# Optimization experiments

Measured on AMD Instinct MI355X. Metric: run time of the kernel, lower is better.

## Reference

```python
import jax, jax.numpy as jnp
import numpy as np

EPS = 1e-6  # flax.linen.LayerNorm default

def layer_norm(x, scale, bias):
    mean = jnp.mean(x, axis=-1, keepdims=True)
    var = jnp.mean(jnp.square(x - mean), axis=-1, keepdims=True)
    return (x - mean) * jax.lax.rsqrt(var + EPS) * scale + bias

def setup_inputs() -> dict:
    key = jax.random.key(0)
    ks = jax.random.split(key, 4)
    B, P, D, H = 2, 2048, 768, 12
    hd = D // H
    x = jax.random.normal(ks[0], (B, P, D), dtype=jnp.float32)
    W_qkv = jax.random.normal(ks[1], (D, 3 * D), dtype=jnp.float32) * (D ** -0.5)
    W_out = jax.random.normal(ks[2], (D, D), dtype=jnp.float32) * (D ** -0.5)
    b_out = jnp.zeros((D,), dtype=jnp.float32)
    return {
        "x": x,
        "W_qkv": W_qkv,
        "q_scale": jnp.ones((hd,), jnp.float32),
        "q_bias": jnp.zeros((hd,), jnp.float32),
        "k_scale": jnp.ones((hd,), jnp.float32),
        "k_bias": jnp.zeros((hd,), jnp.float32),
        "o_scale": jnp.ones((D,), jnp.float32),
        "o_bias": jnp.zeros((D,), jnp.float32),
        "W_out": W_out,
        "b_out": b_out,
    }

def reference(x, W_qkv, q_scale, q_bias, k_scale, k_bias, o_scale, o_bias, W_out, b_out):
    B, P, D = x.shape
    H = 12
    hd = D // H
    scale = hd ** -0.5
    # fused QKV projection, no bias
    qkv = (x @ W_qkv).reshape(B, P, 3, H, hd).transpose(2, 0, 3, 1, 4)  # [3,B,H,P,hd]
    q, k, v = qkv[0], qkv[1], qkv[2]
    # per-head QK LayerNorm over head_dim
    q = layer_norm(q, q_scale, q_bias) * scale
    k = layer_norm(k, k_scale, k_bias)
    attn = jnp.einsum("bhqd,bhkd->bhqk", q, k)
    attn = jax.nn.softmax(attn, axis=-1)
    out = jnp.einsum("bhqk,bhkd->bhqd", attn, v)  # [B,H,P,hd]
    out = jnp.swapaxes(out, 1, 2).reshape(B, P, D)
    out = layer_norm(out, o_scale, o_bias)
    return out @ W_out + b_out
```

## Files before the change

kernel.cpp:

```cpp
#include <hip/hip_runtime.h>
#include <hip/hip_bf16.h>

#define B_  2
#define P_  2048
#define D_  768
#define H_  12
#define HD_ 64
#define M_  (B_ * P_)
#define N1_ (3 * D_)

typedef __attribute__((ext_vector_type(8))) short short8;
typedef __attribute__((ext_vector_type(4))) float f32x4;
typedef __attribute__((ext_vector_type(16))) float f32x16;
typedef unsigned short ushort;

__device__ __forceinline__ ushort f2bf(float f) {
    unsigned u = __float_as_uint(f);
    u += 0x7fffu + ((u >> 16) & 1u);
    return (ushort)(u >> 16);
}

__global__ __launch_bounds__(512) void gemm_qkv_mfma(
        const float* __restrict__ x, const float* __restrict__ w,
        const float* __restrict__ qs, const float* __restrict__ qb,
        const float* __restrict__ ks, const float* __restrict__ kb,
        ushort* __restrict__ qkv) {
    __shared__ __align__(16) ushort As[128][40];
    __shared__ __align__(16) ushort Bs[128][40];

    const int tid  = threadIdx.x;
    const int lane = tid & 63;
    const int wv   = tid >> 6;
    const int quad = lane >> 4;
    const int col  = lane & 15;
    const int wr   = (wv >> 1) * 32;
    const int wc   = (wv & 1) * 64;
    const int rowBase = blockIdx.y * 128;
    const int colBase = blockIdx.x * 128;

    const int am0 = tid >> 3, ac4 = tid & 7;
    const int nB  = tid & 127, kq = tid >> 7;

    float4 apre[2];
    float  bpre[8];
    auto load_tile = [&](int kt) {
        const int k0 = kt * 32;
        apre[0] = *(const float4*)(x + (size_t)(rowBase + am0) * D_ + k0 + ac4 * 4);
        apre[1] = *(const float4*)(x + (size_t)(rowBase + am0 + 64) * D_ + k0 + ac4 * 4);
#pragma unroll
        for (int j = 0; j < 8; j++)
            bpre[j] = w[(size_t)(k0 + kq * 8 + j) * N1_ + colBase + nB];
    };

    f32x4 acc[2][4];
#pragma unroll
    for (int i = 0; i < 2; i++)
#pragma unroll
        for (int j = 0; j < 4; j++) acc[i][j] = (f32x4){0.f, 0.f, 0.f, 0.f};

    load_tile(0);
    const int NT = D_ / 32;
    for (int kt = 0; kt < NT; kt++) {
        __syncthreads();
        {
            ushort u0[4] = {f2bf(apre[0].x), f2bf(apre[0].y), f2bf(apre[0].z), f2bf(apre[0].w)};
            ushort u1[4] = {f2bf(apre[1].x), f2bf(apre[1].y), f2bf(apre[1].z), f2bf(apre[1].w)};
            *(uint2*)&As[am0][ac4 * 4]      = *(uint2*)u0;
            *(uint2*)&As[am0 + 64][ac4 * 4] = *(uint2*)u1;
            ushort us[8];
#pragma unroll
            for (int j = 0; j < 8; j++) us[j] = f2bf(bpre[j]);
            *(short8*)&Bs[nB][kq * 8] = *(short8*)&us[0];
        }
        __syncthreads();
        if (kt + 1 < NT) load_tile(kt + 1);

        short8 af[2], bf[4];
#pragma unroll
        for (int mt = 0; mt < 2; mt++) af[mt] = *(const short8*)&As[wr + mt * 16 + col][quad * 8];
#pragma unroll
        for (int nt = 0; nt < 4; nt++) bf[nt] = *(const short8*)&Bs[wc + nt * 16 + col][quad * 8];
#pragma unroll
        for (int mt = 0; mt < 2; mt++)
#pragma unroll
            for (int nt = 0; nt < 4; nt++)
                acc[mt][nt] = __builtin_amdgcn_mfma_f32_16x16x32_bf16(af[mt], bf[nt], acc[mt][nt], 0, 0, 0);
    }

    const int comp = colBase / D_;
    const int rem  = colBase + wc - comp * D_;
    const int h    = rem >> 6;
    float sc4[4] = {0, 0, 0, 0}, bi4[4] = {0, 0, 0, 0};
    if (comp == 0) {
#pragma unroll
        for (int nt = 0; nt < 4; nt++) { sc4[nt] = qs[nt * 16 + col]; bi4[nt] = qb[nt * 16 + col]; }
    } else if (comp == 1) {
#pragma unroll
        for (int nt = 0; nt < 4; nt++) { sc4[nt] = ks[nt * 16 + col]; bi4[nt] = kb[nt * 16 + col]; }
    }

#pragma unroll
    for (int mt = 0; mt < 2; mt++) {
#pragma unroll
        for (int r = 0; r < 4; r++) {
            int m  = rowBase + wr + mt * 16 + quad * 4 + r;
            int bb = m >> 11;
            int p  = m & 2047;
            float v0 = acc[mt][0][r], v1 = acc[mt][1][r], v2 = acc[mt][2][r], v3 = acc[mt][3][r];
            if (comp < 2) {
                float s = v0 + v1 + v2 + v3;
#pragma unroll
                for (int off = 1; off < 16; off <<= 1) s += __shfl_xor(s, off, 64);
                float mean = s * (1.0f / 64.0f);
                float d0 = v0 - mean, d1 = v1 - mean, d2 = v2 - mean, d3 = v3 - mean;
                float sq = d0 * d0 + d1 * d1 + d2 * d2 + d3 * d3;
#pragma unroll
                for (int off = 1; off < 16; off <<= 1) sq += __shfl_xor(sq, off, 64);
                float inv = rsqrtf(sq * (1.0f / 64.0f) + 1e-6f);
                v0 = d0 * inv * sc4[0] + bi4[0];
                v1 = d1 * inv * sc4[1] + bi4[1];
                v2 = d2 * inv * sc4[2] + bi4[2];
                v3 = d3 * inv * sc4[3] + bi4[3];
                if (comp == 0) { v0 *= 0.125f; v1 *= 0.125f; v2 *= 0.125f; v3 *= 0.125f; }
            }
            size_t base = ((((size_t)comp * B_ + bb) * H_ + h) * P_ + p) * HD_;
            qkv[base +  0 + col] = f2bf(v0);
            qkv[base + 16 + col] = f2bf(v1);
            qkv[base + 32 + col] = f2bf(v2);
            qkv[base + 48 + col] = f2bf(v3);
        }
    }
}

__global__ __launch_bounds__(256) void attn_split(const ushort* __restrict__ qkv,
                                                  float* __restrict__ o0,
                                                  float* __restrict__ o1,
                                                  float* __restrict__ l0,
                                                  float* __restrict__ l1) {
    const int p0 = blockIdx.x * 128;
    const int bh = blockIdx.y;
    const int s  = blockIdx.z;
    const int b  = bh / H_, h = bh % H_;
    float* opart = s ? o1 : o0;
    float* lpart = s ? l1 : l0;
    const int tid  = threadIdx.x;
    const int lane = tid & 63;
    const int wv   = tid >> 6;
    const int half = lane >> 5;
    const int n32  = lane & 31;

    __shared__ __align__(16) ushort Ks[64][72];
    __shared__ __align__(16) ushort Vs[64][72];
    __shared__ __align__(16) ushort Ps[4][32][72];

    const size_t hs = (size_t)P_ * HD_;
    const ushort* qg = qkv + ((size_t)(0 * B_ + b) * H_ + h) * hs + (size_t)(p0 + wv * 32) * HD_;
    const ushort* kg = qkv + ((size_t)(1 * B_ + b) * H_ + h) * hs + (size_t)s * (P_ / 2) * HD_;
    const ushort* vg = qkv + ((size_t)(2 * B_ + b) * H_ + h) * hs + (size_t)s * (P_ / 2) * HD_;

    short8 aq[4];
#pragma unroll
    for (int ks2 = 0; ks2 < 4; ks2++)
        aq[ks2] = *(const short8*)(qg + (size_t)n32 * HD_ + ks2 * 16 + half * 8);

    float lrow[16];
#pragma unroll
    for (int r = 0; r < 16; r++) lrow[r] = 0.f;
    f32x16 oacc[2];
#pragma unroll
    for (int nt = 0; nt < 2; nt++)
#pragma unroll
        for (int r = 0; r < 16; r++) oacc[nt][r] = 0.f;

    const int kr = tid >> 3, kc8 = tid & 7;
    const int vd = tid & 63,  vkh = tid >> 6;

    uint4  kpre[2];
    ushort vpre[16];
    auto load_tile = [&](int kt) {
        const ushort* kg_t = kg + (size_t)kt * 64 * HD_;
        const ushort* vg_t = vg + (size_t)kt * 64 * HD_;
        kpre[0] = *(const uint4*)(kg_t + (size_t)kr * HD_ + kc8 * 8);
        kpre[1] = *(const uint4*)(kg_t + (size_t)(kr + 32) * HD_ + kc8 * 8);
#pragma unroll
        for (int j = 0; j < 16; j++)
            vpre[j] = vg_t[(size_t)(vkh * 16 + j) * HD_ + vd];
    };

    load_tile(0);
    const int NT = (P_ / 2) / 64;
    for (int kt = 0; kt < NT; kt++) {
        __syncthreads();
        *(uint4*)&Ks[kr][kc8 * 8]      = kpre[0];
        *(uint4*)&Ks[kr + 32][kc8 * 8] = kpre[1];
        *(short8*)&Vs[vd][vkh * 16]     = *(short8*)&vpre[0];
        *(short8*)&Vs[vd][vkh * 16 + 8] = *(short8*)&vpre[8];
        __syncthreads();
        if (kt + 1 < NT) load_tile(kt + 1);

        f32x16 sc[2];
#pragma unroll
        for (int nt = 0; nt < 2; nt++) {
#pragma unroll
            for (int r = 0; r < 16; r++) sc[nt][r] = 0.f;
#pragma unroll
            for (int ks2 = 0; ks2 < 4; ks2++) {
                short8 kb2 = *(const short8*)&Ks[nt * 32 + n32][ks2 * 16 + half * 8];
                sc[nt] = __builtin_amdgcn_mfma_f32_32x32x16_bf16(aq[ks2], kb2, sc[nt], 0, 0, 0);
            }
        }

#pragma unroll
        for (int reg = 0; reg < 16; reg++) {
            int row = (reg & 3) + 8 * (reg >> 2) + 4 * half;
#pragma unroll
            for (int nt = 0; nt < 2; nt++) {
                float p = __expf(fminf(sc[nt][reg], 60.f));
                lrow[reg] += p;
                Ps[wv][row][nt * 32 + n32] = f2bf(p);
            }
        }

#pragma unroll
        for (int kp = 0; kp < 4; kp++) {
            short8 pa = *(const short8*)&Ps[wv][n32][kp * 16 + half * 8];
#pragma unroll
            for (int nt = 0; nt < 2; nt++) {
                short8 vb = *(const short8*)&Vs[nt * 32 + n32][kp * 16 + half * 8];
                oacc[nt] = __builtin_amdgcn_mfma_f32_32x32x16_bf16(pa, vb, oacc[nt], 0, 0, 0);
            }
        }
    }

#pragma unroll
    for (int reg = 0; reg < 16; reg++) {
#pragma unroll
        for (int off = 1; off < 32; off <<= 1)
            lrow[reg] += __shfl_xor(lrow[reg], off, 64);
    }

    if (n32 == 0) {
#pragma unroll
        for (int reg = 0; reg < 16; reg++) {
            int row = (reg & 3) + 8 * (reg >> 2) + 4 * half;
            lpart[(size_t)bh * P_ + p0 + wv * 32 + row] = lrow[reg];
        }
    }

    float* Psf = (float*)&Ps[wv][0][0];
#pragma unroll
    for (int nt = 0; nt < 2; nt++) {
#pragma unroll
        for (int reg = 0; reg < 16; reg++) {
            int row = (reg & 3) + 8 * (reg >> 2) + 4 * half;
            Psf[row * 36 + n32] = oacc[nt][reg];
        }
#pragma unroll
        for (int i = 0; i < 4; i++) {
            int ql = i * 8 + (lane >> 3);
            int c4 = lane & 7;
            float4 v = *(const float4*)&Psf[ql * 36 + c4 * 4];
            *(float4*)(opart + ((size_t)bh * P_ + p0 + wv * 32 + ql) * HD_ + nt * 32 + c4 * 4) = v;
        }
    }
}

__global__ __launch_bounds__(256) void ln_o(const float* __restrict__ o0,
                                            const float* __restrict__ o1,
                                            const float* __restrict__ l0,
                                            const float* __restrict__ l1,
                                            ushort* __restrict__ lnb,
                                            const float* __restrict__ osc,
                                            const float* __restrict__ ob) {
    __shared__ float red[4];
    __shared__ float red2[4];
    const int row = blockIdx.x;
    const int b   = row >> 11;
    const int p   = row & (P_ - 1);
    const int tid = threadIdx.x;

    auto src = [&](int d) {
        int h = d >> 6;
        size_t lr  = (size_t)(b * H_ + h) * P_ + p;
        size_t idx = lr * HD_ + (d & 63);
        return (o0[idx] + o1[idx]) / (l0[lr] + l1[lr]);
    };
    float v0 = src(tid);
    float v1 = src(tid + 256);
    float v2 = src(tid + 512);
    float s = v0 + v1 + v2;
#pragma unroll
    for (int o = 32; o > 0; o >>= 1) s += __shfl_xor(s, o, 64);
    if ((tid & 63) == 0) red[tid >> 6] = s;
    __syncthreads();
    float mean = (red[0] + red[1] + red[2] + red[3]) * (1.0f / 768.0f);
    float d0 = v0 - mean, d1 = v1 - mean, d2 = v2 - mean;
    float sq = d0 * d0 + d1 * d1 + d2 * d2;
#pragma unroll
    for (int o = 32; o > 0; o >>= 1) sq += __shfl_xor(sq, o, 64);
    if ((tid & 63) == 0) red2[tid >> 6] = sq;
    __syncthreads();
    float var = (red2[0] + red2[1] + red2[2] + red2[3]) * (1.0f / 768.0f);
    float inv = rsqrtf(var + 1e-6f);
    const size_t base = (size_t)row * D_;
    lnb[base + tid]       = f2bf(d0 * inv * osc[tid]       + ob[tid]);
    lnb[base + tid + 256] = f2bf(d1 * inv * osc[tid + 256] + ob[tid + 256]);
    lnb[base + tid + 512] = f2bf(d2 * inv * osc[tid + 512] + ob[tid + 512]);
}

__global__ __launch_bounds__(256) void gemm_out_mfma(
        const ushort* __restrict__ a, const float* __restrict__ w,
        const float* __restrict__ bias, float* __restrict__ out) {
    __shared__ __align__(16) ushort As[64][40];
    __shared__ __align__(16) ushort Bs[64][40];

    const int tid  = threadIdx.x;
    const int lane = tid & 63;
    const int wv   = tid >> 6;
    const int quad = lane >> 4;
    const int col  = lane & 15;
    const int wr   = (wv >> 1) * 32;
    const int wc   = (wv & 1) * 32;
    const int rowBase = blockIdx.y * 64;
    const int colBase = blockIdx.x * 64;

    const int am  = tid >> 2, ac8 = tid & 3;
    const int nB  = tid & 63, kq = tid >> 6;

    uint4 apre;
    float bpre[8];
    auto load_tile = [&](int kt) {
        const int k0 = kt * 32;
        apre = *(const uint4*)(a + (size_t)(rowBase + am) * D_ + k0 + ac8 * 8);
#pragma unroll
        for (int j = 0; j < 8; j++)
            bpre[j] = w[(size_t)(k0 + kq * 8 + j) * D_ + colBase + nB];
    };

    f32x4 acc[2][2];
#pragma unroll
    for (int i = 0; i < 2; i++)
#pragma unroll
        for (int j = 0; j < 2; j++) acc[i][j] = (f32x4){0.f, 0.f, 0.f, 0.f};

    load_tile(0);
    const int NT = D_ / 32;
    for (int kt = 0; kt < NT; kt++) {
        __syncthreads();
        *(uint4*)&As[am][ac8 * 8] = apre;
        {
            ushort us[8];
#pragma unroll
            for (int j = 0; j < 8; j++) us[j] = f2bf(bpre[j]);
            *(short8*)&Bs[nB][kq * 8] = *(short8*)&us[0];
        }
        __syncthreads();
        if (kt + 1 < NT) load_tile(kt + 1);

        short8 af[2], bf[2];
#pragma unroll
        for (int mt = 0; mt < 2; mt++) af[mt] = *(const short8*)&As[wr + mt * 16 + col][quad * 8];
#pragma unroll
        for (int nt = 0; nt < 2; nt++) bf[nt] = *(const short8*)&Bs[wc + nt * 16 + col][quad * 8];
#pragma unroll
        for (int mt = 0; mt < 2; mt++)
#pragma unroll
            for (int nt = 0; nt < 2; nt++)
                acc[mt][nt] = __builtin_amdgcn_mfma_f32_16x16x32_bf16(af[mt], bf[nt], acc[mt][nt], 0, 0, 0);
    }

    float b2[2];
#pragma unroll
    for (int nt = 0; nt < 2; nt++) b2[nt] = bias[colBase + wc + nt * 16 + col];
#pragma unroll
    for (int mt = 0; mt < 2; mt++) {
#pragma unroll
        for (int r = 0; r < 4; r++) {
            int m = rowBase + wr + mt * 16 + quad * 4 + r;
            float* dst = out + (size_t)m * D_ + colBase + wc;
#pragma unroll
            for (int nt = 0; nt < 2; nt++)
                dst[nt * 16 + col] = acc[mt][nt][r] + b2[nt];
        }
    }
}

extern "C" void kernel_launch(void* const* d_in, const int* in_sizes, int n_in,
                              void* d_out, int out_size, void* d_ws, size_t ws_size,
                              hipStream_t stream) {
    const float* x    = (const float*)d_in[0];
    const float* Wqkv = (const float*)d_in[1];
    const float* qs   = (const float*)d_in[2];
    const float* qb   = (const float*)d_in[3];
    const float* ks   = (const float*)d_in[4];
    const float* kb   = (const float*)d_in[5];
    const float* osc  = (const float*)d_in[6];
    const float* ob   = (const float*)d_in[7];
    const float* Wout = (const float*)d_in[8];
    const float* bout = (const float*)d_in[9];
    float* out = (float*)d_out;

    ushort* qkv    = (ushort*)d_ws;
    float*  opart0 = (float*)(qkv + (size_t)3 * B_ * H_ * P_ * HD_);
    float*  l0     = opart0 + (size_t)B_ * H_ * P_ * HD_;
    float*  l1     = l0 + (size_t)B_ * H_ * P_;
    float*  opart1 = out;
    ushort* ln_buf = qkv;

    gemm_qkv_mfma<<<dim3(N1_ / 128, M_ / 128), 512, 0, stream>>>(x, Wqkv, qs, qb, ks, kb, qkv);
    attn_split<<<dim3(P_ / 128, B_ * H_, 2), 256, 0, stream>>>(qkv, opart0, opart1, l0, l1);
    ln_o<<<dim3(M_), 256, 0, stream>>>(opart0, opart1, l0, l1, ln_buf, osc, ob);
    gemm_out_mfma<<<dim3(D_ / 64, M_ / 64), 256, 0, stream>>>(ln_buf, Wout, bout, out);
}
```

Baseline: 214.6 us.

## Keep softmax probabilities in registers via transposed MFMA and split KV four ways

The attention kernel now computes S^T by swapping MFMA operands, so each lane's exp'd scores can be packed directly into the B-operand of the PV MFMA. This removes the per-wave LDS round trip for P and the final cross-lane row-sum reduction, and K rows are written to LDS with a swapped row order to match the new layout. When the workspace is large enough, the KV dimension is split four ways instead of two to raise grid parallelism, at the cost of more partial output traffic that the LN kernel must sum.

```diff
diff --git a/kernel.cpp b/kernel.cpp
--- a/kernel.cpp
+++ b/kernel.cpp
@@ -12,12 +12,21 @@
 typedef __attribute__((ext_vector_type(8))) short short8;
 typedef __attribute__((ext_vector_type(4))) float f32x4;
 typedef __attribute__((ext_vector_type(16))) float f32x16;
+typedef __attribute__((ext_vector_type(4))) unsigned u32x4;
 typedef unsigned short ushort;
 
 __device__ __forceinline__ ushort f2bf(float f) {
     unsigned u = __float_as_uint(f);
     u += 0x7fffu + ((u >> 16) & 1u);
     return (ushort)(u >> 16);
+}
+
+__device__ __forceinline__ unsigned pk2bf(float a, float b) {
+    return (unsigned)f2bf(a) | ((unsigned)f2bf(b) << 16);
+}
+
+__device__ __forceinline__ int swap23(int s) {
+    return (s & ~12) | ((s & 4) << 1) | ((s & 8) >> 1);
 }
 
 __global__ __launch_bounds__(512) void gemm_qkv_mfma(
@@ -133,46 +142,47 @@
 }
 
 __global__ __launch_bounds__(256) void attn_split(const ushort* __restrict__ qkv,
-                                                  float* __restrict__ o0,
-                                                  float* __restrict__ o1,
-                                                  float* __restrict__ l0,
-                                                  float* __restrict__ l1) {
-    const int p0 = blockIdx.x * 128;
-    const int bh = blockIdx.y;
-    const int s  = blockIdx.z;
-    const int b  = bh / H_, h = bh % H_;
-    float* opart = s ? o1 : o0;
-    float* lpart = s ? l1 : l0;
+                                                  float* __restrict__ o0, float* __restrict__ o1,
+                                                  float* __restrict__ o2, float* __restrict__ o3,
+                                                  float* __restrict__ l0, float* __restrict__ l1,
+                                                  float* __restrict__ l2, float* __restrict__ l3) {
+    const int p0  = blockIdx.x * 128;
+    const int bh  = blockIdx.y;
+    const int s   = blockIdx.z;
+    const int nsp = gridDim.z;
+    const int b   = bh / H_, h = bh % H_;
+    float* opart = (s == 0) ? o0 : (s == 1) ? o1 : (s == 2) ? o2 : o3;
+    float* lpart = (s == 0) ? l0 : (s == 1) ? l1 : (s == 2) ? l2 : l3;
     const int tid  = threadIdx.x;
     const int lane = tid & 63;
     const int wv   = tid >> 6;
     const int half = lane >> 5;
     const int n32  = lane & 31;
 
-    __shared__ __align__(16) ushort Ks[64][72];
-    __shared__ __align__(16) ushort Vs[64][72];
-    __shared__ __align__(16) ushort Ps[4][32][72];
-
-    const size_t hs = (size_t)P_ * HD_;
+    __shared__ __align__(16) ushort KVs[2][64][72];
+    ushort (&Ks)[64][72] = KVs[0];
+    ushort (&Vs)[64][72] = KVs[1];
+
+    const size_t hs  = (size_t)P_ * HD_;
+    const int    kv0 = s * (P_ / nsp);
     const ushort* qg = qkv + ((size_t)(0 * B_ + b) * H_ + h) * hs + (size_t)(p0 + wv * 32) * HD_;
-    const ushort* kg = qkv + ((size_t)(1 * B_ + b) * H_ + h) * hs + (size_t)s * (P_ / 2) * HD_;
-    const ushort* vg = qkv + ((size_t)(2 * B_ + b) * H_ + h) * hs + (size_t)s * (P_ / 2) * HD_;
+    const ushort* kg = qkv + ((size_t)(1 * B_ + b) * H_ + h) * hs + (size_t)kv0 * HD_;
+    const ushort* vg = qkv + ((size_t)(2 * B_ + b) * H_ + h) * hs + (size_t)kv0 * HD_;
 
     short8 aq[4];
 #pragma unroll
     for (int ks2 = 0; ks2 < 4; ks2++)
         aq[ks2] = *(const short8*)(qg + (size_t)n32 * HD_ + ks2 * 16 + half * 8);
 
-    float lrow[16];
-#pragma unroll
-    for (int r = 0; r < 16; r++) lrow[r] = 0.f;
-    f32x16 oacc[2];
+    float lsum = 0.f;
+    f32x16 oaccT[2];
 #pragma unroll
     for (int nt = 0; nt < 2; nt++)
 #pragma unroll
-        for (int r = 0; r < 16; r++) oacc[nt][r] = 0.f;
+        for (int r = 0; r < 16; r++) oaccT[nt][r] = 0.f;
 
     const int kr = tid >> 3, kc8 = tid & 7;
+    const int krs = swap23(kr);
     const int vd = tid & 63,  vkh = tid >> 6;
 
     uint4  kpre[2];
@@ -188,87 +198,81 @@
     };
 
     load_tile(0);
-    const int NT = (P_ / 2) / 64;
+    const int NT = (P_ / 64) / nsp;
     for (int kt = 0; kt < NT; kt++) {
         __syncthreads();
-        *(uint4*)&Ks[kr][kc8 * 8]      = kpre[0];
-        *(uint4*)&Ks[kr + 32][kc8 * 8] = kpre[1];
+        *(uint4*)&Ks[krs][kc8 * 8]      = kpre[0];
+        *(uint4*)&Ks[krs + 32][kc8 * 8] = kpre[1];
         *(short8*)&Vs[vd][vkh * 16]     = *(short8*)&vpre[0];
         *(short8*)&Vs[vd][vkh * 16 + 8] = *(short8*)&vpre[8];
         __syncthreads();
         if (kt + 1 < NT) load_tile(kt + 1);
 
-        f32x16 sc[2];
+        u32x4 pw[2][2];
 #pragma unroll
         for (int nt = 0; nt < 2; nt++) {
-#pragma unroll
-            for (int r = 0; r < 16; r++) sc[nt][r] = 0.f;
+            f32x16 sc;
+#pragma unroll
+            for (int r = 0; r < 16; r++) sc[r] = 0.f;
 #pragma unroll
             for (int ks2 = 0; ks2 < 4; ks2++) {
                 short8 kb2 = *(const short8*)&Ks[nt * 32 + n32][ks2 * 16 + half * 8];
-                sc[nt] = __builtin_amdgcn_mfma_f32_32x32x16_bf16(aq[ks2], kb2, sc[nt], 0, 0, 0);
+                sc = __builtin_amdgcn_mfma_f32_32x32x16_bf16(kb2, aq[ks2], sc, 0, 0, 0);
             }
-        }
-
-#pragma unroll
-        for (int reg = 0; reg < 16; reg++) {
-            int row = (reg & 3) + 8 * (reg >> 2) + 4 * half;
-#pragma unroll
-            for (int nt = 0; nt < 2; nt++) {
-                float p = __expf(fminf(sc[nt][reg], 60.f));
-                lrow[reg] += p;
-                Ps[wv][row][nt * 32 + n32] = f2bf(p);
+            float p[16];
+#pragma unroll
+            for (int r = 0; r < 16; r++) {
+                p[r] = __expf(fminf(sc[r], 60.f));
+                lsum += p[r];
             }
-        }
-
-#pragma unroll
-        for (int kp = 0; kp < 4; kp++) {
-            short8 pa = *(const short8*)&Ps[wv][n32][kp * 16 + half * 8];
-#pragma unroll
-            for (int nt = 0; nt < 2; nt++) {
-                short8 vb = *(const short8*)&Vs[nt * 32 + n32][kp * 16 + half * 8];
-                oacc[nt] = __builtin_amdgcn_mfma_f32_32x32x16_bf16(pa, vb, oacc[nt], 0, 0, 0);
+#pragma unroll
+            for (int kp2 = 0; kp2 < 2; kp2++)
+#pragma unroll
+                for (int i = 0; i < 4; i++)
+                    pw[nt][kp2][i] = pk2bf(p[kp2 * 8 + 2 * i], p[kp2 * 8 + 2 * i + 1]);
+        }
+
+#pragma unroll
+        for (int kstep = 0; kstep < 4; kstep++) {
+            short8 pb = __builtin_bit_cast(short8, pw[kstep >> 1][kstep & 1]);
+#pragma unroll
+            for (int ntd = 0; ntd < 2; ntd++) {
+                short8 av = *(const short8*)&Vs[ntd * 32 + n32][kstep * 16 + half * 8];
+                oaccT[ntd] = __builtin_amdgcn_mfma_f32_32x32x16_bf16(av, pb, oaccT[ntd], 0, 0, 0);
             }
         }
     }
 
-#pragma unroll
-    for (int reg = 0; reg < 16; reg++) {
-#pragma unroll
-        for (int off = 1; off < 32; off <<= 1)
-            lrow[reg] += __shfl_xor(lrow[reg], off, 64);
-    }
-
-    if (n32 == 0) {
-#pragma unroll
-        for (int reg = 0; reg < 16; reg++) {
-            int row = (reg & 3) + 8 * (reg >> 2) + 4 * half;
-            lpart[(size_t)bh * P_ + p0 + wv * 32 + row] = lrow[reg];
-        }
-    }
-
-    float* Psf = (float*)&Ps[wv][0][0];
-#pragma unroll
-    for (int nt = 0; nt < 2; nt++) {
-#pragma unroll
-        for (int reg = 0; reg < 16; reg++) {
-            int row = (reg & 3) + 8 * (reg >> 2) + 4 * half;
-            Psf[row * 36 + n32] = oacc[nt][reg];
-        }
+    lsum += __shfl_xor(lsum, 32, 64);
+    if (lane < 32)
+        lpart[(size_t)bh * P_ + p0 + wv * 32 + lane] = lsum;
+
+    __syncthreads();
+    float* scr = (float*)&KVs[0][0][0] + wv * 1152;
+#pragma unroll
+    for (int ntd = 0; ntd < 2; ntd++) {
+#pragma unroll
+        for (int r = 0; r < 16; r++)
+            scr[n32 * 36 + (r & 3) + 8 * (r >> 2) + 4 * half] = oaccT[ntd][r];
 #pragma unroll
         for (int i = 0; i < 4; i++) {
             int ql = i * 8 + (lane >> 3);
             int c4 = lane & 7;
-            float4 v = *(const float4*)&Psf[ql * 36 + c4 * 4];
-            *(float4*)(opart + ((size_t)bh * P_ + p0 + wv * 32 + ql) * HD_ + nt * 32 + c4 * 4) = v;
+            float4 v = *(const float4*)&scr[ql * 36 + c4 * 4];
+            *(float4*)(opart + ((size_t)bh * P_ + p0 + wv * 32 + ql) * HD_ + ntd * 32 + c4 * 4) = v;
         }
     }
 }
 
 __global__ __launch_bounds__(256) void ln_o(const float* __restrict__ o0,
                                             const float* __restrict__ o1,
+                                            const float* __restrict__ o2,
+                                            const float* __restrict__ o3,
                                             const float* __restrict__ l0,
                                             const float* __restrict__ l1,
+                                            const float* __restrict__ l2,
+                                            const float* __restrict__ l3,
+                                            const int ns,
                                             ushort* __restrict__ lnb,
                                             const float* __restrict__ osc,
                                             const float* __restrict__ ob) {
@@ -283,7 +287,10 @@
         int h = d >> 6;
         size_t lr  = (size_t)(b * H_ + h) * P_ + p;
         size_t idx = lr * HD_ + (d & 63);
-        return (o0[idx] + o1[idx]) / (l0[lr] + l1[lr]);
+        float num = o0[idx] + o1[idx];
+        float den = l0[lr] + l1[lr];
+        if (ns == 4) { num += o2[idx] + o3[idx]; den += l2[lr] + l3[lr]; }
+        return num / den;
     };
     float v0 = src(tid);
     float v1 = src(tid + 256);
@@ -400,15 +407,29 @@
     const float* bout = (const float*)d_in[9];
     float* out = (float*)d_out;
 
-    ushort* qkv    = (ushort*)d_ws;
-    float*  opart0 = (float*)(qkv + (size_t)3 * B_ * H_ * P_ * HD_);
-    float*  l0     = opart0 + (size_t)B_ * H_ * P_ * HD_;
-    float*  l1     = l0 + (size_t)B_ * H_ * P_;
-    float*  opart1 = out;
+    ushort* qkv = (ushort*)d_ws;
+    const size_t qkvE = (size_t)3 * B_ * H_ * P_ * HD_;
+    const size_t oE   = (size_t)B_ * H_ * P_ * HD_;
+    const size_t lE   = (size_t)B_ * H_ * P_;
+    float* base = (float*)(qkv + qkvE);
+    const size_t need4 = qkvE * sizeof(ushort) + (3 * oE + 4 * lE) * sizeof(float);
+    const int nsp = (ws_size >= need4) ? 4 : 2;
+    float* op[4];
+    float* lbase;
+    if (nsp == 4) {
+        op[0] = base; op[1] = base + oE; op[2] = base + 2 * oE; op[3] = out;
+        lbase = base + 3 * oE;
+    } else {
+        op[0] = base; op[1] = out; op[2] = base; op[3] = base;
+        lbase = base + oE;
+    }
+    float* lp[4] = {lbase, lbase + lE, lbase + 2 * lE, lbase + 3 * lE};
     ushort* ln_buf = qkv;
 
     gemm_qkv_mfma<<<dim3(N1_ / 128, M_ / 128), 512, 0, stream>>>(x, Wqkv, qs, qb, ks, kb, qkv);
-    attn_split<<<dim3(P_ / 128, B_ * H_, 2), 256, 0, stream>>>(qkv, opart0, opart1, l0, l1);
-    ln_o<<<dim3(M_), 256, 0, stream>>>(opart0, opart1, l0, l1, ln_buf, osc, ob);
+    attn_split<<<dim3(P_ / 128, B_ * H_, nsp), 256, 0, stream>>>(
+        qkv, op[0], op[1], op[2], op[3], lp[0], lp[1], lp[2], lp[3]);
+    ln_o<<<dim3(M_), 256, 0, stream>>>(
+        op[0], op[1], op[2], op[3], lp[0], lp[1], lp[2], lp[3], nsp, ln_buf, osc, ob);
     gemm_out_mfma<<<dim3(D_ / 64, M_ / 64), 256, 0, stream>>>(ln_buf, Wout, bout, out);
 }
```

Result: faster. 209.4 us (-2.4%).
